# Performance work log

Measured on AMD Instinct MI355X. Metric: run time of the kernel, lower is better.

The kernel has to match this reference:

```python
import jax, jax.numpy as jnp
import numpy as np

B, S, D = 1, 2048, 2048
H, DH = 16, 128
GEMMA2_TANH_SCALE = 50.0


def _rotate_half(x):
    x1, x2 = jnp.split(x, 2, axis=-1)
    return jnp.concatenate([-x2, x1], axis=-1)


def setup_inputs() -> dict:
    key = jax.random.key(0)
    ks = jax.random.split(key, 8)
    x = jax.random.normal(ks[0], (B, S, D), dtype=jnp.float32)
    # rotary tables per position: cos/sin of theta_i duplicated over half-dim pairs
    inv_freq = 1.0 / (10000.0 ** (jnp.arange(0, DH // 2, dtype=jnp.float32) / (DH // 2)))
    t = jnp.arange(S, dtype=jnp.float32)
    freqs = jnp.einsum('s,d->sd', t, inv_freq)          # [S, DH/2]
    emb = jnp.concatenate([freqs, freqs], axis=-1)       # [S, DH]
    rope_cos = jnp.cos(emb)
    rope_sin = jnp.sin(emb)
    # causal additive mask [1,1,S,S]
    neg = jnp.float32(-1e9)
    mask = jnp.where(jnp.tril(jnp.ones((S, S), dtype=bool)), 0.0, neg)[None, None]
    scale = 1.0 / np.sqrt(D)
    wq = jax.random.normal(ks[1], (H * DH, D), dtype=jnp.float32) * scale
    wk = jax.random.normal(ks[2], (H * DH, D), dtype=jnp.float32) * scale
    wv = jax.random.normal(ks[3], (H * DH, D), dtype=jnp.float32) * scale
    wo = jax.random.normal(ks[4], (D, H * DH), dtype=jnp.float32) * scale
    return {"x": x, "rope_cos": rope_cos, "rope_sin": rope_sin, "mask": mask,
            "wq": wq, "wk": wk, "wv": wv, "wo": wo}


def reference(x, rope_cos, rope_sin, mask, wq, wk, wv, wo):
    b, s, _ = x.shape
    xq = jnp.einsum('bsd,pd->bsp', x, wq).reshape(b, s, H, DH)
    xk = jnp.einsum('bsd,pd->bsp', x, wk).reshape(b, s, H, DH)
    xv = jnp.einsum('bsd,pd->bsp', x, wv).reshape(b, s, H, DH)
    cos = rope_cos[None, :, None, :]  # [1,S,1,DH]
    sin = rope_sin[None, :, None, :]
    xq = xq * cos + _rotate_half(xq) * sin
    xk = xk * cos + _rotate_half(xk) * sin
    q = xq.transpose(0, 2, 1, 3)  # [B,H,S,DH]
    k = xk.transpose(0, 2, 1, 3)
    v = xv.transpose(0, 2, 1, 3)
    scores = jnp.einsum('bhqd,bhkd->bhqk', q, k) / np.sqrt(DH)
    scores = jnp.tanh(scores / GEMMA2_TANH_SCALE) * GEMMA2_TANH_SCALE
    scores = scores + mask
    probs = jax.nn.softmax(scores.astype(jnp.float32), axis=-1).astype(q.dtype)
    out = jnp.einsum('bhqk,bhkd->bhqd', probs, v)
    out = out.transpose(0, 2, 1, 3).reshape(b, s, H * DH)
    return jnp.einsum('bsp,dp->bsd', out, wo)
```

## Files before the change

### kernel.cpp

```cpp
#include <hip/hip_runtime.h>

#define SS 2048
#define DD 2048
#define HH 16
#define DHD 128

#define SCORE_SCALE 0.08838834764831845f
#define C2 0.0035355339059327377f

typedef unsigned short u16;
typedef __attribute__((ext_vector_type(8))) short short8;
typedef __attribute__((ext_vector_type(4))) short short4v;
typedef __attribute__((ext_vector_type(4))) float f32x4;

__device__ __forceinline__ float bf2f(u16 v) {
  union { unsigned u; float f; } x; x.u = ((unsigned)v) << 16; return x.f;
}
__device__ __forceinline__ u16 f2bf(float f) {
  union { float f; unsigned u; } x; x.f = f;
  unsigned r = (x.u + 0x7fffu + ((x.u >> 16) & 1u)) >> 16;
  return (u16)r;
}

#define GL2LDS16(g, l) __builtin_amdgcn_global_load_lds( \
    (const __attribute__((address_space(1))) void*)(g),   \
    (__attribute__((address_space(3))) void*)(l), 16, 0, 0)

__global__ __launch_bounds__(256) void cvt_bf16(const float* __restrict__ in,
                                                u16* __restrict__ out) {
  int i = (blockIdx.x * 256 + threadIdx.x) * 8;
  float4 a = *(const float4*)(in + i);
  float4 b = *(const float4*)(in + i + 4);
  short8 o;
  o[0] = (short)f2bf(a.x); o[1] = (short)f2bf(a.y);
  o[2] = (short)f2bf(a.z); o[3] = (short)f2bf(a.w);
  o[4] = (short)f2bf(b.x); o[5] = (short)f2bf(b.y);
  o[6] = (short)f2bf(b.z); o[7] = (short)f2bf(b.w);
  *(short8*)(out + i) = o;
}


#define GEMM_STAGE(Asrc, Bsrc, Adst, Bdst, kofs)                               \
  _Pragma("unroll")                                                            \
  for (int half = 0; half < 2; ++half) {                                       \
    const int rb = half * 64 + wave * 16;                                      \
    GL2LDS16(Asrc + (size_t)(bm + rb + lrow) * DD + (kofs) + c8s, Adst + rb * 32); \
    GL2LDS16(Bsrc + (size_t)(bn + rb + lrow) * DD + (kofs) + c8s, Bdst + rb * 32); \
  }

#define GEMM_COMPUTE(Abuf, Bbuf)                                               \
  {                                                                            \
    short8 af[4], bb[4];                                                       \
    _Pragma("unroll")                                                          \
    for (int m = 0; m < 4; ++m) {                                              \
      const int row = wm + m * 16 + fr;                                        \
      af[m] = *(const short8*)(Abuf + row * 32 + (hi ^ (row & 3)) * 8);        \
    }                                                                          \
    _Pragma("unroll")                                                          \
    for (int n = 0; n < 4; ++n) {                                              \
      const int row = wn + n * 16 + fr;                                        \
      bb[n] = *(const short8*)(Bbuf + row * 32 + (hi ^ (row & 3)) * 8);        \
    }                                                                          \
    __builtin_amdgcn_s_setprio(1);                                             \
    _Pragma("unroll")                                                          \
    for (int m = 0; m < 4; ++m)                                                \
      _Pragma("unroll")                                                        \
      for (int n = 0; n < 4; ++n)                                              \
        acc[m][n] = __builtin_amdgcn_mfma_f32_16x16x32_bf16(af[m], bb[n], acc[m][n], 0, 0, 0); \
    __builtin_amdgcn_s_setprio(0);                                             \
  }

template<typename OUT, bool TR>
__global__ __launch_bounds__(256) void gemm_bt(const u16* __restrict__ A,
                                               const u16* __restrict__ B,
                                               OUT* __restrict__ C) {
  __shared__ u16 As[2][128 * 32];
  __shared__ u16 Bs[2][128 * 32];
  const int tid = threadIdx.x, wave = tid >> 6, lane = tid & 63;
  const int wm = (wave >> 1) * 64, wn = (wave & 1) * 64;
  const int bm = blockIdx.y * 128, bn = blockIdx.x * 128;
  const int lrow = lane >> 2;
  const int c8s = ((lane & 3) ^ (lrow & 3)) * 8;
  const int fr = lane & 15, hi = lane >> 4, fq4 = hi * 4;
  f32x4 acc[4][4] = {};
  GEMM_STAGE(A, B, As[0], Bs[0], 0)
  __syncthreads();
  for (int kt = 0; kt < DD / 32; ++kt) {
    const int buf = kt & 1;
    if (kt + 1 < DD / 32) { GEMM_STAGE(A, B, As[buf ^ 1], Bs[buf ^ 1], (kt + 1) * 32) }
    GEMM_COMPUTE(As[buf], Bs[buf])
    __syncthreads();
  }
#pragma unroll
  for (int m = 0; m < 4; ++m)
#pragma unroll
    for (int n = 0; n < 4; ++n) {
      const int row0 = bm + wm + m * 16 + fq4;
      const int col  = bn + wn + n * 16 + fr;
      if constexpr (TR) {
        short4v t;
#pragma unroll
        for (int r = 0; r < 4; ++r) t[r] = (short)f2bf(acc[m][n][r]);
        *(short4v*)((u16*)C + (size_t)col * SS + row0) = t;
      } else {
#pragma unroll
        for (int r = 0; r < 4; ++r) {
          if constexpr (sizeof(OUT) == 2)
            ((u16*)C)[(size_t)(row0 + r) * DD + col] = f2bf(acc[m][n][r]);
          else
            ((float*)C)[(size_t)(row0 + r) * DD + col] = acc[m][n][r];
        }
      }
    }
}

__global__ __launch_bounds__(256) void gemm_qkv(const u16* __restrict__ A,
                                                const u16* __restrict__ Bq,
                                                const u16* __restrict__ Bk,
                                                const u16* __restrict__ Bv,
                                                u16* __restrict__ Cq,
                                                u16* __restrict__ Ck,
                                                u16* __restrict__ Cvt) {
  __shared__ u16 As[2][128 * 32];
  __shared__ u16 Bs[2][128 * 32];
  const int z = blockIdx.z;
  const u16* B = (z == 0) ? Bq : (z == 1) ? Bk : Bv;
  const int tid = threadIdx.x, wave = tid >> 6, lane = tid & 63;
  const int wm = (wave >> 1) * 64, wn = (wave & 1) * 64;
  const int bm = blockIdx.y * 128, bn = blockIdx.x * 128;
  const int lrow = lane >> 2;
  const int c8s = ((lane & 3) ^ (lrow & 3)) * 8;
  const int fr = lane & 15, hi = lane >> 4, fq4 = hi * 4;
  f32x4 acc[4][4] = {};
  GEMM_STAGE(A, B, As[0], Bs[0], 0)
  __syncthreads();
  for (int kt = 0; kt < DD / 32; ++kt) {
    const int buf = kt & 1;
    if (kt + 1 < DD / 32) { GEMM_STAGE(A, B, As[buf ^ 1], Bs[buf ^ 1], (kt + 1) * 32) }
    GEMM_COMPUTE(As[buf], Bs[buf])
    __syncthreads();
  }
  u16* Cn = (z == 0) ? Cq : Ck;
#pragma unroll
  for (int m = 0; m < 4; ++m)
#pragma unroll
    for (int n = 0; n < 4; ++n) {
      const int row0 = bm + wm + m * 16 + fq4;
      const int col  = bn + wn + n * 16 + fr;
      if (z < 2) {
#pragma unroll
        for (int r = 0; r < 4; ++r)
          Cn[(size_t)(row0 + r) * DD + col] = f2bf(acc[m][n][r]);
      } else {
        short4v t;
#pragma unroll
        for (int r = 0; r < 4; ++r) t[r] = (short)f2bf(acc[m][n][r]);
        *(short4v*)(Cvt + (size_t)col * SS + row0) = t;
      }
    }
}

__global__ __launch_bounds__(128) void rope_qk(const u16* __restrict__ qin,
                                               const u16* __restrict__ kin,
                                               const float* __restrict__ cosd,
                                               const float* __restrict__ sind,
                                               u16* __restrict__ qt,
                                               u16* __restrict__ kt) {
  const int s = blockIdx.x, h = blockIdx.y, d = threadIdx.x;
  const float c = cosd[s * DHD + d], sn = sind[s * DHD + d];
  const int base = s * DD + h * DHD;
  const float q0 = bf2f(qin[base + d]);
  const float k0 = bf2f(kin[base + d]);
  const float qr = (d < 64) ? -bf2f(qin[base + d + 64]) : bf2f(qin[base + d - 64]);
  const float kr = (d < 64) ? -bf2f(kin[base + d + 64]) : bf2f(kin[base + d - 64]);
  const size_t o = ((size_t)h * SS + s) * DHD + d;
  qt[o] = f2bf(q0 * c + qr * sn);
  kt[o] = f2bf(k0 * c + kr * sn);
}

__global__ __launch_bounds__(256) void attn_fwd(const u16* __restrict__ qt,
                                                const u16* __restrict__ kt,
                                                const u16* __restrict__ vt,
                                                u16* __restrict__ ao) {
  __shared__ u16 Ks[2][64 * 128];
  __shared__ u16 Vs[2][128 * 64];
  __shared__ u16 Ps[4][16 * 64];
  const int bid = blockIdx.x;
  const int h  = (bid & 7) + 8 * ((bid >> 3) & 1);
  const int qb = (SS / 64 - 1) - (bid >> 4);
  const int tid = threadIdx.x, wave = tid >> 6, lane = tid & 63;
  const int q0 = qb * 64 + wave * 16;
  const int fr = lane & 15, hi = lane >> 4, fq8 = hi * 8, fq4 = hi * 4;

  const int kbrow0 = wave * 4 + (lane >> 4);
  const int kc8    = (lane & 15);
  const int vbrow0 = wave * 8 + (lane >> 3);
  const int vk8    = (lane & 7) ^ ((lane >> 3) & 7);

  short8 qf[4];
#pragma unroll
  for (int c = 0; c < 4; ++c)
    qf[c] = *(const short8*)(qt + ((size_t)h * SS + q0 + fr) * DHD + c * 32 + fq8);

  f32x4 oacc[8] = {};
  float lsum[4] = {0.f, 0.f, 0.f, 0.f};

  const int nt = qb + 1;

  auto STAGE = [&](int t, int buf) {
    const int kb = t * 64;
#pragma unroll
    for (int i = 0; i < 4; ++i) {
      const int krow = i * 16 + kbrow0;
      const int c8 = kc8 ^ (krow & 7);
      GL2LDS16(kt + ((size_t)h * SS + kb + krow) * DHD + c8 * 8,
               &Ks[buf][(i * 16 + wave * 4) * 128]);
    }
#pragma unroll
    for (int i = 0; i < 4; ++i) {
      const int vrow = i * 32 + vbrow0;
      GL2LDS16(vt + ((size_t)h * DHD + vrow) * SS + kb + vk8 * 8,
               &Vs[buf][(i * 32 + wave * 8) * 64]);
    }
  };

  STAGE(0, 0);
  __syncthreads();

  for (int t = 0; t < nt; ++t) {
    const int buf = t & 1;
    if (t + 1 < nt) STAGE(t + 1, buf ^ 1);
    const int kb = t * 64;

    f32x4 sacc[4] = {};
    __builtin_amdgcn_s_setprio(1);
#pragma unroll
    for (int n = 0; n < 4; ++n) {
      const int row = n * 16 + fr;
#pragma unroll
      for (int c = 0; c < 4; ++c) {
        short8 b = *(const short8*)(&Ks[buf][row * 128 + ((c * 4 + hi) ^ (fr & 7)) * 8]);
        sacc[n] = __builtin_amdgcn_mfma_f32_16x16x32_bf16(qf[c], b, sacc[n], 0, 0, 0);
      }
    }
    __builtin_amdgcn_s_setprio(0);

    const bool diag = (t == nt - 1);
    float p[4][4];
#pragma unroll
    for (int n = 0; n < 4; ++n)
#pragma unroll
      for (int r = 0; r < 4; ++r) {
        const float w = __expf(sacc[n][r] * C2);
        float pv = __expf(-100.0f * __builtin_amdgcn_rcpf(1.0f + w));
        if (diag) {
          const int kg = kb + n * 16 + fr;
          if (kg > q0 + fq4 + r) pv = 0.0f;
        }
        p[n][r] = pv;
        lsum[r] += pv;
      }

    u16* ps = &Ps[wave][0];
#pragma unroll
    for (int n = 0; n < 4; ++n)
#pragma unroll
      for (int r = 0; r < 4; ++r) {
        const int prow = fq4 + r;
        const int chunk = n * 2 + (fr >> 3);
        ps[prow * 64 + ((chunk ^ (prow & 7)) << 3) + (fr & 7)] = f2bf(p[n][r]);
      }
    short8 pa[2];
#pragma unroll
    for (int kc = 0; kc < 2; ++kc)
      pa[kc] = *(const short8*)(ps + fr * 64 + (((kc * 4 + hi) ^ (fr & 7)) << 3));

    __builtin_amdgcn_s_setprio(1);
#pragma unroll
    for (int kc = 0; kc < 2; ++kc)
#pragma unroll
      for (int n = 0; n < 8; ++n) {
        const int row = n * 16 + fr;
        short8 b = *(const short8*)(&Vs[buf][row * 64 + (((kc * 4 + hi) ^ (fr & 7)) << 3)]);
        oacc[n] = __builtin_amdgcn_mfma_f32_16x16x32_bf16(pa[kc], b, oacc[n], 0, 0, 0);
      }
    __builtin_amdgcn_s_setprio(0);
    __syncthreads();
  }

  float rl[4];
#pragma unroll
  for (int r = 0; r < 4; ++r) {
    float v = lsum[r];
    v += __shfl_xor(v, 1); v += __shfl_xor(v, 2);
    v += __shfl_xor(v, 4); v += __shfl_xor(v, 8);
    rl[r] = 1.0f / v;
  }
#pragma unroll
  for (int n = 0; n < 8; ++n)
#pragma unroll
    for (int r = 0; r < 4; ++r) {
      const float v = oacc[n][r] * rl[r];
      ao[(size_t)(q0 + fq4 + r) * DD + h * DHD + n * 16 + fr] = f2bf(v);
    }
}

extern "C" void kernel_launch(void* const* d_in, const int* in_sizes, int n_in,
                              void* d_out, int out_size, void* d_ws, size_t ws_size,
                              hipStream_t stream) {
  const float* x        = (const float*)d_in[0];
  const float* rope_cos = (const float*)d_in[1];
  const float* rope_sin = (const float*)d_in[2];
  const float* wq = (const float*)d_in[4];
  const float* wk = (const float*)d_in[5];
  const float* wv = (const float*)d_in[6];
  const float* wo = (const float*)d_in[7];
  float* out = (float*)d_out;

  u16* ws = (u16*)d_ws;
  const size_t SZ = (size_t)SS * DD;
  u16* xb  = ws + 0 * SZ;
  u16* wqb = ws + 1 * SZ;
  u16* wkb = ws + 2 * SZ;
  u16* wvb = ws + 3 * SZ;
  u16* q_  = ws + 4 * SZ;
  u16* k_  = ws + 5 * SZ;
  u16* vt  = ws + 6 * SZ;
  u16* qt  = wqb;
  u16* kt  = wkb;
  u16* ao  = wvb;
  u16* wob = q_;

  const int cvtGrid = (int)(SZ / (256 * 8));
  cvt_bf16<<<cvtGrid, 256, 0, stream>>>(x,  xb);
  cvt_bf16<<<cvtGrid, 256, 0, stream>>>(wq, wqb);
  cvt_bf16<<<cvtGrid, 256, 0, stream>>>(wk, wkb);
  cvt_bf16<<<cvtGrid, 256, 0, stream>>>(wv, wvb);

  gemm_qkv<<<dim3(16, 16, 3), 256, 0, stream>>>(xb, wqb, wkb, wvb, q_, k_, vt);

  rope_qk<<<dim3(SS, HH), 128, 0, stream>>>(q_, k_, rope_cos, rope_sin, qt, kt);

  cvt_bf16<<<cvtGrid, 256, 0, stream>>>(wo, wob);

  attn_fwd<<<512, 256, 0, stream>>>(qt, kt, vt, ao);

  gemm_bt<float, false><<<dim3(16, 16), 256, 0, stream>>>(ao, wob, out);
}
```

Before: 320.7 us.

## Fuse RoPE into QKV GEMM epilogue, merge conversions, change LDS swizzle

Moves the rotary embedding into the Q/K GEMM epilogue: each tile is staged through LDS and written with RoPE already applied in head-major layout, so the separate rope kernel and its round trip of Q/K through global memory go away. The five fp32-to-bf16 conversion launches become a single 2D launch. The LDS swizzle changes to XOR with (row>>1)&3 to alter the bank-conflict pattern, and the k-loop is manually unrolled by two with fixed buffer pointers. Costs are extra LDS and a sync in the QKV epilogue, plus a larger workspace (eight buffers instead of seven).

```diff
diff --git a/kernel.cpp b/kernel.cpp
--- a/kernel.cpp
+++ b/kernel.cpp
@@ -26,8 +26,17 @@
     (const __attribute__((address_space(1))) void*)(g),   \
     (__attribute__((address_space(3))) void*)(l), 16, 0, 0)
 
-__global__ __launch_bounds__(256) void cvt_bf16(const float* __restrict__ in,
-                                                u16* __restrict__ out) {
+__global__ __launch_bounds__(256) void cvt5(const float* __restrict__ i0,
+                                            const float* __restrict__ i1,
+                                            const float* __restrict__ i2,
+                                            const float* __restrict__ i3,
+                                            const float* __restrict__ i4,
+                                            u16* __restrict__ o0, u16* __restrict__ o1,
+                                            u16* __restrict__ o2, u16* __restrict__ o3,
+                                            u16* __restrict__ o4) {
+  const int z = blockIdx.y;
+  const float* in = (z == 0) ? i0 : (z == 1) ? i1 : (z == 2) ? i2 : (z == 3) ? i3 : i4;
+  u16* out = (z == 0) ? o0 : (z == 1) ? o1 : (z == 2) ? o2 : (z == 3) ? o3 : o4;
   int i = (blockIdx.x * 256 + threadIdx.x) * 8;
   float4 a = *(const float4*)(in + i);
   float4 b = *(const float4*)(in + i + 4);
@@ -54,12 +63,12 @@
     _Pragma("unroll")                                                          \
     for (int m = 0; m < 4; ++m) {                                              \
       const int row = wm + m * 16 + fr;                                        \
-      af[m] = *(const short8*)(Abuf + row * 32 + (hi ^ (row & 3)) * 8);        \
+      af[m] = *(const short8*)(Abuf + row * 32 + (hi ^ ((row >> 1) & 3)) * 8); \
     }                                                                          \
     _Pragma("unroll")                                                          \
     for (int n = 0; n < 4; ++n) {                                              \
       const int row = wn + n * 16 + fr;                                        \
-      bb[n] = *(const short8*)(Bbuf + row * 32 + (hi ^ (row & 3)) * 8);        \
+      bb[n] = *(const short8*)(Bbuf + row * 32 + (hi ^ ((row >> 1) & 3)) * 8); \
     }                                                                          \
     __builtin_amdgcn_s_setprio(1);                                             \
     _Pragma("unroll")                                                          \
@@ -70,47 +79,41 @@
     __builtin_amdgcn_s_setprio(0);                                             \
   }
 
-template<typename OUT, bool TR>
+#define GEMM_KLOOP(A_, B_)                                                     \
+  GEMM_STAGE(A_, B_, As0, Bs0, 0)                                              \
+  __syncthreads();                                                             \
+  for (int kk = 0; kk < DD / 32; kk += 2) {                                    \
+    if (kk + 1 < DD / 32) { GEMM_STAGE(A_, B_, As1, Bs1, (kk + 1) * 32) }      \
+    GEMM_COMPUTE(As0, Bs0)                                                     \
+    __syncthreads();                                                           \
+    if (kk + 2 < DD / 32) { GEMM_STAGE(A_, B_, As0, Bs0, (kk + 2) * 32) }      \
+    GEMM_COMPUTE(As1, Bs1)                                                     \
+    __syncthreads();                                                           \
+  }
+
 __global__ __launch_bounds__(256) void gemm_bt(const u16* __restrict__ A,
                                                const u16* __restrict__ B,
-                                               OUT* __restrict__ C) {
-  __shared__ u16 As[2][128 * 32];
-  __shared__ u16 Bs[2][128 * 32];
+                                               float* __restrict__ C) {
+  __shared__ u16 smem[16384];
+  u16* As0 = smem;            u16* As1 = smem + 4096;
+  u16* Bs0 = smem + 8192;     u16* Bs1 = smem + 12288;
   const int tid = threadIdx.x, wave = tid >> 6, lane = tid & 63;
   const int wm = (wave >> 1) * 64, wn = (wave & 1) * 64;
   const int bm = blockIdx.y * 128, bn = blockIdx.x * 128;
   const int lrow = lane >> 2;
-  const int c8s = ((lane & 3) ^ (lrow & 3)) * 8;
+  const int c8s = ((lane & 3) ^ ((lrow >> 1) & 3)) * 8;
   const int fr = lane & 15, hi = lane >> 4, fq4 = hi * 4;
   f32x4 acc[4][4] = {};
-  GEMM_STAGE(A, B, As[0], Bs[0], 0)
-  __syncthreads();
-  for (int kt = 0; kt < DD / 32; ++kt) {
-    const int buf = kt & 1;
-    if (kt + 1 < DD / 32) { GEMM_STAGE(A, B, As[buf ^ 1], Bs[buf ^ 1], (kt + 1) * 32) }
-    GEMM_COMPUTE(As[buf], Bs[buf])
-    __syncthreads();
-  }
+  GEMM_KLOOP(A, B)
 #pragma unroll
   for (int m = 0; m < 4; ++m)
 #pragma unroll
     for (int n = 0; n < 4; ++n) {
       const int row0 = bm + wm + m * 16 + fq4;
       const int col  = bn + wn + n * 16 + fr;
-      if constexpr (TR) {
-        short4v t;
-#pragma unroll
-        for (int r = 0; r < 4; ++r) t[r] = (short)f2bf(acc[m][n][r]);
-        *(short4v*)((u16*)C + (size_t)col * SS + row0) = t;
-      } else {
-#pragma unroll
-        for (int r = 0; r < 4; ++r) {
-          if constexpr (sizeof(OUT) == 2)
-            ((u16*)C)[(size_t)(row0 + r) * DD + col] = f2bf(acc[m][n][r]);
-          else
-            ((float*)C)[(size_t)(row0 + r) * DD + col] = acc[m][n][r];
-        }
-      }
+#pragma unroll
+      for (int r = 0; r < 4; ++r)
+        C[(size_t)(row0 + r) * DD + col] = acc[m][n][r];
     }
 }
 
@@ -118,64 +121,78 @@
                                                 const u16* __restrict__ Bq,
                                                 const u16* __restrict__ Bk,
                                                 const u16* __restrict__ Bv,
-                                                u16* __restrict__ Cq,
-                                                u16* __restrict__ Ck,
-                                                u16* __restrict__ Cvt) {
-  __shared__ u16 As[2][128 * 32];
-  __shared__ u16 Bs[2][128 * 32];
+                                                const float* __restrict__ cosd,
+                                                const float* __restrict__ sind,
+                                                u16* __restrict__ qt,
+                                                u16* __restrict__ kt,
+                                                u16* __restrict__ vt) {
+  __shared__ u16 smem[18432];
+  u16* As0 = smem;            u16* As1 = smem + 4096;
+  u16* Bs0 = smem + 8192;     u16* Bs1 = smem + 12288;
   const int z = blockIdx.z;
   const u16* B = (z == 0) ? Bq : (z == 1) ? Bk : Bv;
   const int tid = threadIdx.x, wave = tid >> 6, lane = tid & 63;
   const int wm = (wave >> 1) * 64, wn = (wave & 1) * 64;
   const int bm = blockIdx.y * 128, bn = blockIdx.x * 128;
   const int lrow = lane >> 2;
-  const int c8s = ((lane & 3) ^ (lrow & 3)) * 8;
+  const int c8s = ((lane & 3) ^ ((lrow >> 1) & 3)) * 8;
   const int fr = lane & 15, hi = lane >> 4, fq4 = hi * 4;
   f32x4 acc[4][4] = {};
-  GEMM_STAGE(A, B, As[0], Bs[0], 0)
+  GEMM_KLOOP(A, B)
+
+  if (z == 2) {
+#pragma unroll
+    for (int m = 0; m < 4; ++m)
+#pragma unroll
+      for (int n = 0; n < 4; ++n) {
+        const int row0 = bm + wm + m * 16 + fq4;
+        const int col  = bn + wn + n * 16 + fr;
+        short4v t;
+#pragma unroll
+        for (int r = 0; r < 4; ++r) t[r] = (short)f2bf(acc[m][n][r]);
+        *(short4v*)(vt + (size_t)col * SS + row0) = t;
+      }
+    return;
+  }
+
+  u16* Ct = smem;
+#pragma unroll
+  for (int m = 0; m < 4; ++m)
+#pragma unroll
+    for (int n = 0; n < 4; ++n) {
+      const int rrow = wm + m * 16 + fq4;
+      const int col  = wn + n * 16 + fr;
+#pragma unroll
+      for (int r = 0; r < 4; ++r)
+        Ct[(rrow + r) * 136 + col] = f2bf(acc[m][n][r]);
+    }
   __syncthreads();
-  for (int kt = 0; kt < DD / 32; ++kt) {
-    const int buf = kt & 1;
-    if (kt + 1 < DD / 32) { GEMM_STAGE(A, B, As[buf ^ 1], Bs[buf ^ 1], (kt + 1) * 32) }
-    GEMM_COMPUTE(As[buf], Bs[buf])
-    __syncthreads();
-  }
-  u16* Cn = (z == 0) ? Cq : Ck;
-#pragma unroll
-  for (int m = 0; m < 4; ++m)
-#pragma unroll
-    for (int n = 0; n < 4; ++n) {
-      const int row0 = bm + wm + m * 16 + fq4;
-      const int col  = bn + wn + n * 16 + fr;
-      if (z < 2) {
-#pragma unroll
-        for (int r = 0; r < 4; ++r)
-          Cn[(size_t)(row0 + r) * DD + col] = f2bf(acc[m][n][r]);
-      } else {
-        short4v t;
-#pragma unroll
-        for (int r = 0; r < 4; ++r) t[r] = (short)f2bf(acc[m][n][r]);
-        *(short4v*)(Cvt + (size_t)col * SS + row0) = t;
-      }
-    }
-}
-
-__global__ __launch_bounds__(128) void rope_qk(const u16* __restrict__ qin,
-                                               const u16* __restrict__ kin,
-                                               const float* __restrict__ cosd,
-                                               const float* __restrict__ sind,
-                                               u16* __restrict__ qt,
-                                               u16* __restrict__ kt) {
-  const int s = blockIdx.x, h = blockIdx.y, d = threadIdx.x;
-  const float c = cosd[s * DHD + d], sn = sind[s * DHD + d];
-  const int base = s * DD + h * DHD;
-  const float q0 = bf2f(qin[base + d]);
-  const float k0 = bf2f(kin[base + d]);
-  const float qr = (d < 64) ? -bf2f(qin[base + d + 64]) : bf2f(qin[base + d - 64]);
-  const float kr = (d < 64) ? -bf2f(kin[base + d + 64]) : bf2f(kin[base + d - 64]);
-  const size_t o = ((size_t)h * SS + s) * DHD + d;
-  qt[o] = f2bf(q0 * c + qr * sn);
-  kt[o] = f2bf(k0 * c + kr * sn);
+
+  const int row  = tid >> 1;
+  const int half = tid & 1;
+  const int d0   = half * 64;
+  const int srow = bm + row;
+  const int head = blockIdx.x;
+  const float sgn = half ? 1.0f : -1.0f;
+  u16* dst = (z == 0) ? qt : kt;
+#pragma unroll
+  for (int j = 0; j < 8; ++j) {
+    const int d = d0 + j * 8;
+    f32x4 c0 = *(const f32x4*)(cosd + (size_t)srow * DHD + d);
+    f32x4 c1 = *(const f32x4*)(cosd + (size_t)srow * DHD + d + 4);
+    f32x4 s0 = *(const f32x4*)(sind + (size_t)srow * DHD + d);
+    f32x4 s1 = *(const f32x4*)(sind + (size_t)srow * DHD + d + 4);
+    short8 xo = *(const short8*)(Ct + row * 136 + d);
+    short8 xp = *(const short8*)(Ct + row * 136 + (d ^ 64));
+    short8 o;
+#pragma unroll
+    for (int jj = 0; jj < 8; ++jj) {
+      const float c = (jj < 4) ? c0[jj] : c1[jj - 4];
+      const float s = (jj < 4) ? s0[jj] : s1[jj - 4];
+      o[jj] = (short)f2bf(bf2f((u16)xo[jj]) * c + sgn * bf2f((u16)xp[jj]) * s);
+    }
+    *(short8*)(dst + ((size_t)head * SS + srow) * DHD + d) = o;
+  }
 }
 
 __global__ __launch_bounds__(256) void attn_fwd(const u16* __restrict__ qt,
@@ -323,27 +340,19 @@
   u16* wqb = ws + 1 * SZ;
   u16* wkb = ws + 2 * SZ;
   u16* wvb = ws + 3 * SZ;
-  u16* q_  = ws + 4 * SZ;
-  u16* k_  = ws + 5 * SZ;
-  u16* vt  = ws + 6 * SZ;
-  u16* qt  = wqb;
-  u16* kt  = wkb;
-  u16* ao  = wvb;
-  u16* wob = q_;
-
-  const int cvtGrid = (int)(SZ / (256 * 8));
-  cvt_bf16<<<cvtGrid, 256, 0, stream>>>(x,  xb);
-  cvt_bf16<<<cvtGrid, 256, 0, stream>>>(wq, wqb);
-  cvt_bf16<<<cvtGrid, 256, 0, stream>>>(wk, wkb);
-  cvt_bf16<<<cvtGrid, 256, 0, stream>>>(wv, wvb);
-
-  gemm_qkv<<<dim3(16, 16, 3), 256, 0, stream>>>(xb, wqb, wkb, wvb, q_, k_, vt);
-
-  rope_qk<<<dim3(SS, HH), 128, 0, stream>>>(q_, k_, rope_cos, rope_sin, qt, kt);
-
-  cvt_bf16<<<cvtGrid, 256, 0, stream>>>(wo, wob);
+  u16* wob = ws + 4 * SZ;
+  u16* qt  = ws + 5 * SZ;
+  u16* kt  = ws + 6 * SZ;
+  u16* vt  = ws + 7 * SZ;
+  u16* ao  = wqb;
+
+  cvt5<<<dim3((int)(SZ / (256 * 8)), 5), 256, 0, stream>>>(
+      x, wq, wk, wv, wo, xb, wqb, wkb, wvb, wob);
+
+  gemm_qkv<<<dim3(16, 16, 3), 256, 0, stream>>>(
+      xb, wqb, wkb, wvb, rope_cos, rope_sin, qt, kt, vt);
 
   attn_fwd<<<512, 256, 0, stream>>>(qt, kt, vt, ao);
 
-  gemm_bt<float, false><<<dim3(16, 16), 256, 0, stream>>>(ao, wob, out);
-}
+  gemm_bt<<<dim3(16, 16), 256, 0, stream>>>(ao, wob, out);
+}
```

After: 325.0 us. Within noise of the previous version (+1.3%).
